# Kernel tuning notes

Measured on AMD Instinct MI355X. Metric: run time of the kernel, lower is better.

The kernel has to match this reference:

```python
import jax, jax.numpy as jnp
import numpy as np

N_NODES = 50000
N_EDGES = 800000
NUM_HEADS = 4
HEAD_DIM = 32
IN_DIM = 128
NEG_SLOPE = 0.2


def setup_inputs() -> dict:
    key = jax.random.key(0)
    k1, k2, k3, k4, k5, k6 = jax.random.split(key, 6)
    x = jax.random.normal(k1, (N_NODES, IN_DIM), dtype=jnp.float32)
    W = jax.random.normal(k2, (NUM_HEADS * HEAD_DIM, IN_DIM), dtype=jnp.float32) * 0.05
    attn_l = jax.random.normal(k3, (NUM_HEADS, HEAD_DIM), dtype=jnp.float32) * 0.05
    attn_r = jax.random.normal(k4, (NUM_HEADS, HEAD_DIM), dtype=jnp.float32) * 0.05
    src = jax.random.randint(k5, (N_EDGES,), 0, N_NODES, dtype=jnp.int32)
    dst = jnp.sort(jax.random.randint(k6, (N_EDGES,), 0, N_NODES, dtype=jnp.int32))
    return {"x": x, "W": W, "attn_l": attn_l, "attn_r": attn_r, "src": src, "dst": dst}


def reference(x, W, attn_l, attn_r, src, dst):
    N = x.shape[0]
    H, D = attn_l.shape
    # linear projection: [N, H*D] -> [N, H, D]
    feat = (x @ W.T).reshape(N, H, D)
    # per-node attention terms  [N, H]
    el = jnp.einsum('nhd,hd->nh', feat, attn_l)
    er = jnp.einsum('nhd,hd->nh', feat, attn_r)
    # per-edge logits (u_add_v) + leaky relu  [E, H]
    e = el[src] + er[dst]
    e = jnp.where(e > 0, e, NEG_SLOPE * e)
    # edge softmax segmented by destination node
    e_max = jax.ops.segment_max(e, dst, num_segments=N)          # [N, H]
    e_exp = jnp.exp(e - e_max[dst])                              # [E, H]
    denom = jax.ops.segment_sum(e_exp, dst, num_segments=N)     # [N, H]
    alpha = e_exp / denom[dst]                                   # [E, H]
    # attention-weighted neighbor aggregation  [N, H, D]
    out = jax.ops.segment_sum(alpha[:, :, None] * feat[src], dst, num_segments=N)
    return out.reshape(N, H * D)
```

## Files before the change

kernel.cpp:

```cpp
#include <hip/hip_runtime.h>
#include <math.h>

#define NN 50000
#define NE 800000
#define NH 4
#define HD 32
#define FD 128
#define NTILE 3125

typedef __attribute__((ext_vector_type(8))) short short8;
typedef __attribute__((ext_vector_type(4))) float floatx4;

__device__ __forceinline__ unsigned short f2bf(float f) {
    union { float f; unsigned u; } v; v.f = f;
    unsigned u = v.u;
    return (unsigned short)((u + 0x7FFFu + ((u >> 16) & 1u)) >> 16);
}
__device__ __forceinline__ float bf_lo(unsigned u) {
    union { unsigned u; float f; } v; v.u = u << 16; return v.f;
}
__device__ __forceinline__ float bf_hi(unsigned u) {
    union { unsigned u; float f; } v; v.u = u & 0xFFFF0000u; return v.f;
}

__global__ __launch_bounds__(512) void k_gemm_fused(const float* __restrict__ x,
                                                    const float* __restrict__ W,
                                                    const float* __restrict__ al,
                                                    const float* __restrict__ ar,
                                                    unsigned short* __restrict__ feat_bf,
                                                    float* __restrict__ el,
                                                    float* __restrict__ er) {
    __shared__ unsigned short Wl[FD * 136];
    const int tid = threadIdx.x;

    for (int p = tid; p < FD * 64; p += 512) {
        int c = p >> 6, k2 = (p & 63) * 2;
        float2 wv = *(const float2*)&W[c * FD + k2];
        *(unsigned*)&Wl[c * 136 + k2] =
            (unsigned)f2bf(wv.x) | ((unsigned)f2bf(wv.y) << 16);
    }
    __syncthreads();

    const int wv_id = tid >> 6, lane = tid & 63;
    const int col = lane & 15, quad = lane >> 4;

    float alr[8], arr[8];
    #pragma unroll
    for (int ct = 0; ct < 8; ++ct) {
        alr[ct] = al[col + 16 * ct];
        arr[ct] = ar[col + 16 * ct];
    }

    for (int tile = blockIdx.x * 8 + wv_id; tile < NTILE; tile += gridDim.x * 8) {
        const int n0 = tile * 16;

        short8 afrag[4];
        const float* xrow = x + (size_t)(n0 + col) * FD;
        #pragma unroll
        for (int s = 0; s < 4; ++s) {
            float4 u0 = *(const float4*)&xrow[s * 32 + quad * 8];
            float4 u1 = *(const float4*)&xrow[s * 32 + quad * 8 + 4];
            short8 a;
            a[0] = (short)f2bf(u0.x); a[1] = (short)f2bf(u0.y);
            a[2] = (short)f2bf(u0.z); a[3] = (short)f2bf(u0.w);
            a[4] = (short)f2bf(u1.x); a[5] = (short)f2bf(u1.y);
            a[6] = (short)f2bf(u1.z); a[7] = (short)f2bf(u1.w);
            afrag[s] = a;
        }

        floatx4 acc[8];
        #pragma unroll
        for (int ct = 0; ct < 8; ++ct) acc[ct] = (floatx4){0.f, 0.f, 0.f, 0.f};

        #pragma unroll
        for (int ct = 0; ct < 8; ++ct) {
            #pragma unroll
            for (int s = 0; s < 4; ++s) {
                short8 b = *(const short8*)&Wl[(ct * 16 + col) * 136 + s * 32 + quad * 8];
                acc[ct] = __builtin_amdgcn_mfma_f32_16x16x32_bf16(afrag[s], b, acc[ct], 0, 0, 0);
            }
        }

        #pragma unroll
        for (int ct = 0; ct < 8; ++ct) {
            #pragma unroll
            for (int r = 0; r < 4; ++r) {
                feat_bf[(size_t)(n0 + quad * 4 + r) * FD + ct * 16 + col] = f2bf(acc[ct][r]);
            }
        }

        #pragma unroll
        for (int r = 0; r < 4; ++r) {
            float ev[8];
            #pragma unroll
            for (int hh = 0; hh < NH; ++hh) {
                ev[hh]     = acc[2 * hh][r] * alr[2 * hh] + acc[2 * hh + 1][r] * alr[2 * hh + 1];
                ev[4 + hh] = acc[2 * hh][r] * arr[2 * hh] + acc[2 * hh + 1][r] * arr[2 * hh + 1];
            }
            #pragma unroll
            for (int m = 1; m < 16; m <<= 1) {
                #pragma unroll
                for (int j = 0; j < 8; ++j) ev[j] += __shfl_xor(ev[j], m);
            }
            if (col == 0) {
                int n = n0 + quad * 4 + r;
                *(float4*)&el[n * NH] = make_float4(ev[0], ev[1], ev[2], ev[3]);
                *(float4*)&er[n * NH] = make_float4(ev[4], ev[5], ev[6], ev[7]);
            }
        }
    }
}

__global__ void k_edgew(const float* __restrict__ el,
                        const float* __restrict__ er,
                        const int* __restrict__ src,
                        const int* __restrict__ dst,
                        float* __restrict__ wE,
                        int* __restrict__ rows) {
    int e = blockIdx.x * blockDim.x + threadIdx.x;
    if (e >= NE) return;
    int sj = src[e], dj = dst[e];

    if (e == 0) {
        for (int n = 0; n <= dj; ++n) rows[n] = 0;
    } else {
        int prev = dst[e - 1];
        for (int n = prev + 1; n <= dj; ++n) rows[n] = e;
    }
    if (e == NE - 1) {
        for (int n = dj + 1; n <= NN; ++n) rows[n] = NE;
    }

    float4 el4 = *(const float4*)&el[sj * NH];
    float4 er4 = *(const float4*)&er[dj * NH];
    float4 w;
    float lg, z;
    lg = el4.x + er4.x; z = fmaxf(lg, 0.2f * lg); w.x = __expf(z);
    lg = el4.y + er4.y; z = fmaxf(lg, 0.2f * lg); w.y = __expf(z);
    lg = el4.z + er4.z; z = fmaxf(lg, 0.2f * lg); w.z = __expf(z);
    lg = el4.w + er4.w; z = fmaxf(lg, 0.2f * lg); w.w = __expf(z);
    *(float4*)&wE[e * NH] = w;
}

__global__ __launch_bounds__(256) void k_aggregate(const unsigned short* __restrict__ feat_bf,
                                                   const float* __restrict__ wE,
                                                   const int* __restrict__ src,
                                                   const int* __restrict__ rows,
                                                   float* __restrict__ out) {
    const int wave = threadIdx.x >> 6;
    const int lane = threadIdx.x & 63;
    const int n = blockIdx.x * 4 + wave;
    if (n >= NN) return;

    const int s = rows[n], t = rows[n + 1];
    const int q  = lane >> 4;
    const int lp = lane & 15;
    const int h  = lp >> 2;
    const int dimoff = 8 * lp;

    float acc[8] = {0.f, 0.f, 0.f, 0.f, 0.f, 0.f, 0.f, 0.f};
    float den = 0.f;

    for (int e = s; e < t; e += 16) {
        int   sjv[4];
        float wv4[4];
        #pragma unroll
        for (int u = 0; u < 4; ++u) {
            int ei = e + 4 * u + q;
            int ec = (ei < t) ? ei : (t - 1);
            sjv[u] = src[ec];
            wv4[u] = (ei < t) ? wE[ec * NH + h] : 0.f;
        }
        uint4 uvv[4];
        #pragma unroll
        for (int u = 0; u < 4; ++u)
            uvv[u] = *(const uint4*)&feat_bf[(size_t)sjv[u] * FD + dimoff];
        #pragma unroll
        for (int u = 0; u < 4; ++u) {
            float w = wv4[u];
            uint4 uv = uvv[u];
            acc[0] += w * bf_lo(uv.x); acc[1] += w * bf_hi(uv.x);
            acc[2] += w * bf_lo(uv.y); acc[3] += w * bf_hi(uv.y);
            acc[4] += w * bf_lo(uv.z); acc[5] += w * bf_hi(uv.z);
            acc[6] += w * bf_lo(uv.w); acc[7] += w * bf_hi(uv.w);
            den += w;
        }
    }

    #pragma unroll
    for (int m = 16; m < 64; m <<= 1) {
        #pragma unroll
        for (int j = 0; j < 8; ++j) acc[j] += __shfl_xor(acc[j], m);
        den += __shfl_xor(den, m);
    }

    if (q == 0) {
        const float rden = (den > 0.f) ? 1.f / den : 0.f;
        float* op = out + (size_t)n * FD + dimoff;
        *(float4*)op       = make_float4(acc[0] * rden, acc[1] * rden, acc[2] * rden, acc[3] * rden);
        *(float4*)(op + 4) = make_float4(acc[4] * rden, acc[5] * rden, acc[6] * rden, acc[7] * rden);
    }
}

extern "C" void kernel_launch(void* const* d_in, const int* in_sizes, int n_in,
                              void* d_out, int out_size, void* d_ws, size_t ws_size,
                              hipStream_t stream) {
    const float* x  = (const float*)d_in[0];
    const float* W  = (const float*)d_in[1];
    const float* al = (const float*)d_in[2];
    const float* ar = (const float*)d_in[3];
    const int* src  = (const int*)d_in[4];
    const int* dst  = (const int*)d_in[5];
    float* out = (float*)d_out;

    unsigned short* feat_bf = (unsigned short*)d_ws;
    float* el = (float*)(feat_bf + (size_t)NN * FD);
    float* er = el + (size_t)NN * NH;
    int*   rows = (int*)(er + (size_t)NN * NH);
    float* wE = (float*)(((uintptr_t)(rows + NN + 1) + 15) & ~(uintptr_t)15);

    k_gemm_fused<<<256, 512, 0, stream>>>(x, W, al, ar, feat_bf, el, er);
    k_edgew<<<(NE + 255) / 256, 256, 0, stream>>>(el, er, src, dst, wE, rows);
    k_aggregate<<<(NN + 3) / 4, 256, 0, stream>>>(feat_bf, wE, src, rows, out);
}
```

Before: 133.6 us.

## Fold edge-weight kernel into GEMM and aggregate; compute el/er via extra MFMA

Removes the separate edge-weight kernel. The CSR row-offset construction moves into a grid-stride tail of the GEMM kernel, and the per-edge exp weights are recomputed inside the aggregation loop from gathered el and er. The el/er terms come from an extra MFMA against precomputed attn·W vectors instead of shuffle reductions. This drops one launch and the write and reread of the E×H weight buffer. In exchange it adds a scattered el gather per edge, redundant exp work across lanes, and bf16 rounding of the folded attention vectors.

Measured after the change: 138.6 us. 3.7% more time.

```diff
diff --git a/kernel.cpp b/kernel.cpp
--- a/kernel.cpp
+++ b/kernel.cpp
@@ -27,10 +27,13 @@
                                                     const float* __restrict__ W,
                                                     const float* __restrict__ al,
                                                     const float* __restrict__ ar,
+                                                    const int* __restrict__ dst,
                                                     unsigned short* __restrict__ feat_bf,
                                                     float* __restrict__ el,
-                                                    float* __restrict__ er) {
+                                                    float* __restrict__ er,
+                                                    int* __restrict__ rows) {
     __shared__ unsigned short Wl[FD * 136];
+    __shared__ unsigned short ABl[16 * 136];
     const int tid = threadIdx.x;
 
     for (int p = tid; p < FD * 64; p += 512) {
@@ -39,17 +42,22 @@
         *(unsigned*)&Wl[c * 136 + k2] =
             (unsigned)f2bf(wv.x) | ((unsigned)f2bf(wv.y) << 16);
     }
+    for (int p = tid; p < 16 * 128; p += 512) {
+        int j = p >> 7, k = p & 127;
+        float g = 0.f;
+        if (j < 8) {
+            int hh = j & 3;
+            const float* av = (j < 4) ? al : ar;
+            #pragma unroll
+            for (int d = 0; d < 32; ++d)
+                g += av[hh * 32 + d] * W[(size_t)(hh * 32 + d) * FD + k];
+        }
+        ABl[j * 136 + k] = f2bf(g);
+    }
     __syncthreads();
 
     const int wv_id = tid >> 6, lane = tid & 63;
     const int col = lane & 15, quad = lane >> 4;
-
-    float alr[8], arr[8];
-    #pragma unroll
-    for (int ct = 0; ct < 8; ++ct) {
-        alr[ct] = al[col + 16 * ct];
-        arr[ct] = ar[col + 16 * ct];
-    }
 
     for (int tile = blockIdx.x * 8 + wv_id; tile < NTILE; tile += gridDim.x * 8) {
         const int n0 = tile * 16;
@@ -69,6 +77,7 @@
         }
 
         floatx4 acc[8];
+        floatx4 accE = (floatx4){0.f, 0.f, 0.f, 0.f};
         #pragma unroll
         for (int ct = 0; ct < 8; ++ct) acc[ct] = (floatx4){0.f, 0.f, 0.f, 0.f};
 
@@ -80,6 +89,11 @@
                 acc[ct] = __builtin_amdgcn_mfma_f32_16x16x32_bf16(afrag[s], b, acc[ct], 0, 0, 0);
             }
         }
+        #pragma unroll
+        for (int s = 0; s < 4; ++s) {
+            short8 b = *(const short8*)&ABl[col * 136 + s * 32 + quad * 8];
+            accE = __builtin_amdgcn_mfma_f32_16x16x32_bf16(afrag[s], b, accE, 0, 0, 0);
+        }
 
         #pragma unroll
         for (int ct = 0; ct < 8; ++ct) {
@@ -88,62 +102,33 @@
                 feat_bf[(size_t)(n0 + quad * 4 + r) * FD + ct * 16 + col] = f2bf(acc[ct][r]);
             }
         }
-
-        #pragma unroll
-        for (int r = 0; r < 4; ++r) {
-            float ev[8];
-            #pragma unroll
-            for (int hh = 0; hh < NH; ++hh) {
-                ev[hh]     = acc[2 * hh][r] * alr[2 * hh] + acc[2 * hh + 1][r] * alr[2 * hh + 1];
-                ev[4 + hh] = acc[2 * hh][r] * arr[2 * hh] + acc[2 * hh + 1][r] * arr[2 * hh + 1];
-            }
-            #pragma unroll
-            for (int m = 1; m < 16; m <<= 1) {
-                #pragma unroll
-                for (int j = 0; j < 8; ++j) ev[j] += __shfl_xor(ev[j], m);
-            }
-            if (col == 0) {
-                int n = n0 + quad * 4 + r;
-                *(float4*)&el[n * NH] = make_float4(ev[0], ev[1], ev[2], ev[3]);
-                *(float4*)&er[n * NH] = make_float4(ev[4], ev[5], ev[6], ev[7]);
-            }
-        }
-    }
-}
-
-__global__ void k_edgew(const float* __restrict__ el,
-                        const float* __restrict__ er,
-                        const int* __restrict__ src,
-                        const int* __restrict__ dst,
-                        float* __restrict__ wE,
-                        int* __restrict__ rows) {
-    int e = blockIdx.x * blockDim.x + threadIdx.x;
-    if (e >= NE) return;
-    int sj = src[e], dj = dst[e];
-
-    if (e == 0) {
-        for (int n = 0; n <= dj; ++n) rows[n] = 0;
-    } else {
-        int prev = dst[e - 1];
-        for (int n = prev + 1; n <= dj; ++n) rows[n] = e;
-    }
-    if (e == NE - 1) {
-        for (int n = dj + 1; n <= NN; ++n) rows[n] = NE;
-    }
-
-    float4 el4 = *(const float4*)&el[sj * NH];
-    float4 er4 = *(const float4*)&er[dj * NH];
-    float4 w;
-    float lg, z;
-    lg = el4.x + er4.x; z = fmaxf(lg, 0.2f * lg); w.x = __expf(z);
-    lg = el4.y + er4.y; z = fmaxf(lg, 0.2f * lg); w.y = __expf(z);
-    lg = el4.z + er4.z; z = fmaxf(lg, 0.2f * lg); w.z = __expf(z);
-    lg = el4.w + er4.w; z = fmaxf(lg, 0.2f * lg); w.w = __expf(z);
-    *(float4*)&wE[e * NH] = w;
+        if (col < 8) {
+            float* base = (col < 4) ? el : er;
+            int hh = col & 3;
+            #pragma unroll
+            for (int r = 0; r < 4; ++r)
+                base[(n0 + quad * 4 + r) * NH + hh] = accE[r];
+        }
+    }
+
+    const int gsz = gridDim.x * 512;
+    for (int i = blockIdx.x * 512 + tid; i < NE; i += gsz) {
+        int cur = dst[i];
+        if (i == 0) {
+            for (int n = 0; n <= cur; ++n) rows[n] = 0;
+        } else {
+            int prev = dst[i - 1];
+            for (int n = prev + 1; n <= cur; ++n) rows[n] = i;
+        }
+        if (i == NE - 1) {
+            for (int n = cur + 1; n <= NN; ++n) rows[n] = NE;
+        }
+    }
 }
 
 __global__ __launch_bounds__(256) void k_aggregate(const unsigned short* __restrict__ feat_bf,
-                                                   const float* __restrict__ wE,
+                                                   const float* __restrict__ el,
+                                                   const float* __restrict__ er,
                                                    const int* __restrict__ src,
                                                    const int* __restrict__ rows,
                                                    float* __restrict__ out) {
@@ -158,26 +143,31 @@
     const int h  = lp >> 2;
     const int dimoff = 8 * lp;
 
+    const float erh = er[n * NH + h];
+
     float acc[8] = {0.f, 0.f, 0.f, 0.f, 0.f, 0.f, 0.f, 0.f};
     float den = 0.f;
 
     for (int e = s; e < t; e += 16) {
-        int   sjv[4];
-        float wv4[4];
+        int sjv[4];
         #pragma unroll
         for (int u = 0; u < 4; ++u) {
             int ei = e + 4 * u + q;
-            int ec = (ei < t) ? ei : (t - 1);
-            sjv[u] = src[ec];
-            wv4[u] = (ei < t) ? wE[ec * NH + h] : 0.f;
-        }
+            sjv[u] = src[(ei < t) ? ei : (t - 1)];
+        }
+        float elv[4];
+        #pragma unroll
+        for (int u = 0; u < 4; ++u) elv[u] = el[sjv[u] * NH + h];
         uint4 uvv[4];
         #pragma unroll
         for (int u = 0; u < 4; ++u)
             uvv[u] = *(const uint4*)&feat_bf[(size_t)sjv[u] * FD + dimoff];
         #pragma unroll
         for (int u = 0; u < 4; ++u) {
-            float w = wv4[u];
+            int ei = e + 4 * u + q;
+            float lg = elv[u] + erh;
+            float z  = fmaxf(lg, 0.2f * lg);
+            float w  = (ei < t) ? __expf(z) : 0.f;
             uint4 uv = uvv[u];
             acc[0] += w * bf_lo(uv.x); acc[1] += w * bf_hi(uv.x);
             acc[2] += w * bf_lo(uv.y); acc[3] += w * bf_hi(uv.y);
@@ -217,9 +207,7 @@
     float* el = (float*)(feat_bf + (size_t)NN * FD);
     float* er = el + (size_t)NN * NH;
     int*   rows = (int*)(er + (size_t)NN * NH);
-    float* wE = (float*)(((uintptr_t)(rows + NN + 1) + 15) & ~(uintptr_t)15);
-
-    k_gemm_fused<<<256, 512, 0, stream>>>(x, W, al, ar, feat_bf, el, er);
-    k_edgew<<<(NE + 255) / 256, 256, 0, stream>>>(el, er, src, dst, wE, rows);
-    k_aggregate<<<(NN + 3) / 4, 256, 0, stream>>>(feat_bf, wE, src, rows, out);
-}
+
+    k_gemm_fused<<<256, 512, 0, stream>>>(x, W, al, ar, dst, feat_bf, el, er, rows);
+    k_aggregate<<<(NN + 3) / 4, 256, 0, stream>>>(feat_bf, el, er, src, rows, out);
+}
```
